# Optimization experiments

Hardware: AMD Instinct MI355X
Metric: run time of the kernel (lower is better)

## Reference

```python
import jax, jax.numpy as jnp
import numpy as np

B = 65536
NFIELD = 20
NFEAT = 1_000_000
SQL_NEMB = 10
DATA_NEMB = 10
HID = 64
K = 16
C = 2
COL_CARD = NFIELD + NFEAT + 1
GATE_IN = NFIELD * SQL_NEMB
EXP_IN = NFIELD * DATA_NEMB
EPS = 1e-5


def _bn(x, g, b, m, v):
    # eval-mode BatchNorm1d: affine normalize with running stats
    return (x - m) * jax.lax.rsqrt(v + EPS) * g + b


def setup_inputs() -> dict:
    key = jax.random.key(0)
    ks = jax.random.split(key, 12)
    n = lambda k, s, sc=0.05: jax.random.normal(k, s, jnp.float32) * sc
    return {
        "x": jax.random.randint(ks[0], (B, NFIELD), 0, NFEAT, dtype=jnp.int32),
        "sql": jax.random.randint(ks[1], (B, NFIELD), 0, COL_CARD, dtype=jnp.int32),
        "input_table": n(ks[2], (NFEAT, DATA_NEMB)),
        "sql_table": n(ks[3], (COL_CARD, SQL_NEMB)),
        "gate_w1": n(ks[4], (GATE_IN, HID)), "gate_b1": jnp.zeros((HID,), jnp.float32),
        "gate_w2": n(ks[5], (HID, K)), "gate_b2": jnp.zeros((K,), jnp.float32),
        "e_w1": n(ks[6], (K, EXP_IN, HID)), "e_b1": jnp.zeros((K, HID), jnp.float32),
        "e_g1": jnp.ones((K, HID), jnp.float32), "e_beta1": jnp.zeros((K, HID), jnp.float32),
        "e_m1": jnp.zeros((K, HID), jnp.float32), "e_v1": jnp.ones((K, HID), jnp.float32),
        "e_w2": n(ks[7], (K, HID, HID)), "e_b2": jnp.zeros((K, HID), jnp.float32),
        "e_g2": jnp.ones((K, HID), jnp.float32), "e_beta2": jnp.zeros((K, HID), jnp.float32),
        "e_m2": jnp.zeros((K, HID), jnp.float32), "e_v2": jnp.ones((K, HID), jnp.float32),
        "p_w1": n(ks[8], (HID, HID)), "p_b1": jnp.zeros((HID,), jnp.float32),
        "p_g": jnp.ones((HID,), jnp.float32), "p_beta": jnp.zeros((HID,), jnp.float32),
        "p_m": jnp.zeros((HID,), jnp.float32), "p_v": jnp.ones((HID,), jnp.float32),
        "p_w2": n(ks[9], (HID, 1)), "p_b2": jnp.zeros((1,), jnp.float32),
    }


def reference(x, sql, input_table, sql_table, gate_w1, gate_b1, gate_w2, gate_b2,
              e_w1, e_b1, e_g1, e_beta1, e_m1, e_v1,
              e_w2, e_b2, e_g2, e_beta2, e_m2, e_v2,
              p_w1, p_b1, p_g, p_beta, p_m, p_v, p_w2, p_b2):
    Bn = x.shape[0]
    # embedding lookups -> flatten fields
    x_emb = input_table[x].reshape(Bn, -1)      # [B, nfield*data_nemb]
    sql_emb = sql_table[sql].reshape(Bn, -1)    # [B, nfield*sql_nemb]
    # gate network (MLP + softmax) over K experts
    gh = jax.nn.relu(sql_emb @ gate_w1 + gate_b1)
    scores = jax.nn.softmax(gh @ gate_w2 + gate_b2, axis=-1)  # [B, K]
    # sparse top-C selection, scatter back to dense gates, renormalize
    topv, topi = jax.lax.top_k(scores, C)
    gates = jnp.zeros_like(scores).at[jnp.arange(Bn)[:, None], topi].set(topv)
    gates = gates / (gates.sum(-1, keepdims=True) + 1e-9)     # [B, K]
    # expert compute (dense-equivalent; zero gates kill unselected experts)
    h1 = jax.nn.relu(_bn(jnp.einsum('bi,kih->kbh', x_emb, e_w1) + e_b1[:, None, :],
                         e_g1[:, None, :], e_beta1[:, None, :], e_m1[:, None, :], e_v1[:, None, :]))
    h2 = jax.nn.relu(_bn(jnp.einsum('kbh,khg->kbg', h1, e_w2) + e_b2[:, None, :],
                         e_g2[:, None, :], e_beta2[:, None, :], e_m2[:, None, :], e_v2[:, None, :]))
    y = jnp.einsum('bk,kbh->bh', gates, h2)                   # combine [B, HID]
    # load-balance loss: cv^2 of expert importance
    importance = gates.sum(0)
    loss = importance.var() / (importance.mean() ** 2 + 1e-10)
    # predict head
    ph = jax.nn.relu(_bn(y @ p_w1 + p_b1, p_g, p_beta, p_m, p_v))
    out = (ph @ p_w2 + p_b2).squeeze(-1)                      # [B]
    return out, loss
```

## Files before the change

### kernel.cpp

```cpp
#include <hip/hip_runtime.h>
#include <hip/hip_bf16.h>

#define BB 65536
#define NFIELD 20
#define HID 64
#define KEXP 16
#define EPS 1e-5f
#define KPAD 224
#define NKS 7
#define NBLK_GATE 1024
#define NBX_EXP 40
#define TSTR 228

typedef __attribute__((ext_vector_type(8))) short v8s;
typedef __attribute__((ext_vector_type(4))) float v4f;

#define OFF_GCNT 0
#define OFF_SC1 64
#define OFF_SH1 1088
#define OFF_SC2 2112
#define OFF_SH2 3136
#define OFF_SCP 4160
#define OFF_SHP 4224
#define OFF_IMP 4288
#define OFF_LIDX 20672
#define OFF_LW  1069248
#define OFF_W1T 2117824
#define OFF_GW1T 2232512
#define OFF_W2T 2239680
#define OFF_PW1T 2272448
#define OFF_XEMB 2274496
#define OFF_HS 9614640

__device__ __forceinline__ unsigned short f2bf(float f) {
    unsigned int u = __float_as_uint(f);
    unsigned int r = (u + 0x7FFFu + ((u >> 16) & 1u)) >> 16;
    return (unsigned short)r;
}
__device__ __forceinline__ float bf2f(unsigned short u) {
    unsigned int t = ((unsigned int)u) << 16;
    return __uint_as_float(t);
}
__device__ __forceinline__ unsigned int pack2(float a, float b) {
    return (unsigned int)f2bf(a) | ((unsigned int)f2bf(b) << 16);
}

__global__ __launch_bounds__(256) void k_prep(
    const float* __restrict__ ew1, const float* __restrict__ ew2,
    const float* __restrict__ gw1, const float* __restrict__ pw1,
    const float* __restrict__ eb1, const float* __restrict__ eg1,
    const float* __restrict__ ebe1, const float* __restrict__ em1,
    const float* __restrict__ ev1,
    const float* __restrict__ eb2, const float* __restrict__ eg2,
    const float* __restrict__ ebe2, const float* __restrict__ em2,
    const float* __restrict__ ev2,
    const float* __restrict__ pb1, const float* __restrict__ pg,
    const float* __restrict__ pbe, const float* __restrict__ pm,
    const float* __restrict__ pv,
    float* __restrict__ wsf, int* __restrict__ gcnt,
    unsigned short* __restrict__ w1t, unsigned short* __restrict__ gw1t,
    unsigned short* __restrict__ w2t, unsigned short* __restrict__ pw1t)
{
    int gid = blockIdx.x * 256 + threadIdx.x;
    if (gid < 229376) {
        int k = gid / 14336, r = gid % 14336, c = r / KPAD, t = r % KPAD;
        w1t[gid] = (t < 200) ? f2bf(ew1[((size_t)k * 200 + t) * HID + c]) : 0;
    } else if (gid < 229376 + 14336) {
        int g2 = gid - 229376; int c = g2 / KPAD, t = g2 % KPAD;
        gw1t[g2] = (t < 200) ? f2bf(gw1[t * HID + c]) : 0;
    } else if (gid < 243712 + 65536) {
        int g2 = gid - 243712; int k = g2 / 4096, r = g2 % 4096, g = r / 64, i = r % 64;
        w2t[g2] = f2bf(ew2[((size_t)k * 64 + i) * 64 + g]);
    } else if (gid < 309248 + 4096) {
        int g2 = gid - 309248; int g = g2 / 64, i = g2 % 64;
        pw1t[g2] = f2bf(pw1[i * 64 + g]);
    } else if (gid < 313344 + 1024) {
        int t = gid - 313344;
        float rs1 = rsqrtf(ev1[t] + EPS) * eg1[t];
        wsf[OFF_SC1 + t] = rs1;
        wsf[OFF_SH1 + t] = fmaf(eb1[t] - em1[t], rs1, ebe1[t]);
        float rs2 = rsqrtf(ev2[t] + EPS) * eg2[t];
        wsf[OFF_SC2 + t] = rs2;
        wsf[OFF_SH2 + t] = fmaf(eb2[t] - em2[t], rs2, ebe2[t]);
    } else if (gid < 314368 + 64) {
        int t = gid - 314368;
        float rs = rsqrtf(pv[t] + EPS) * pg[t];
        wsf[OFF_SCP + t] = rs;
        wsf[OFF_SHP + t] = fmaf(pb1[t] - pm[t], rs, pbe[t]);
    } else if (gid < 314432 + 16) {
        gcnt[gid - 314432] = 0;
    }
}

__global__ __launch_bounds__(256) void k_gate(
    const int* __restrict__ x, const int* __restrict__ sql,
    const float* __restrict__ itab, const float* __restrict__ stab,
    const unsigned short* __restrict__ gw1t,
    const float* __restrict__ gb1, const float* __restrict__ gw2,
    const float* __restrict__ gb2,
    unsigned short* __restrict__ xembT,
    int* __restrict__ lidx, float* __restrict__ lw,
    int* __restrict__ gcnt, float* __restrict__ imp_part)
{
    __shared__ unsigned short tile[64][TSTR];
    __shared__ float s_imp[KEXP];
    __shared__ int s_cnt[KEXP];
    __shared__ int s_base[KEXP];
    unsigned short (*Hg)[80] = (unsigned short (*)[80])&tile[0][0];
    int tid = threadIdx.x;
    int wid = tid >> 6, l = tid & 63;
    int m = l & 15, q = l >> 4;
    int b0 = blockIdx.x * 64;

    if (tid < KEXP) { s_imp[tid] = 0.f; s_cnt[tid] = 0; }
    for (int t = tid; t < 64 * 12; t += 256) {
        int r = t / 12, c2 = t % 12;
        *(unsigned int*)&tile[r][200 + 2 * c2] = 0;
    }
    {
        uint4 z4 = {0u, 0u, 0u, 0u};
        if (tid < 192) {
            int row = tid / 3, j = tid % 3;
            *(uint4*)((char*)(xembT + (size_t)(b0 + row) * KPAD) + 400 + 16 * j) = z4;
        }
    }
#pragma unroll
    for (int rr = 0; rr < 5; ++rr) {
        int r = tid + rr * 256;
        int lb = r / NFIELD, f = r % NFIELD;
        int sidx = sql[(size_t)(b0 + lb) * NFIELD + f];
        int xidx = x[(size_t)(b0 + lb) * NFIELD + f];
        const float* srow = stab + (size_t)sidx * 10;
        const float* xrow = itab + (size_t)xidx * 10;
        float2 s0 = *(const float2*)(srow + 0);
        float2 s1 = *(const float2*)(srow + 2);
        float2 s2 = *(const float2*)(srow + 4);
        float2 s3 = *(const float2*)(srow + 6);
        float2 s4 = *(const float2*)(srow + 8);
        float2 x0 = *(const float2*)(xrow + 0);
        float2 x1 = *(const float2*)(xrow + 2);
        float2 x2 = *(const float2*)(xrow + 4);
        float2 x3 = *(const float2*)(xrow + 6);
        float2 x4 = *(const float2*)(xrow + 8);
        unsigned int* lrow = (unsigned int*)&tile[lb][f * 10];
        lrow[0] = pack2(s0.x, s0.y);
        lrow[1] = pack2(s1.x, s1.y);
        lrow[2] = pack2(s2.x, s2.y);
        lrow[3] = pack2(s3.x, s3.y);
        lrow[4] = pack2(s4.x, s4.y);
        unsigned int* grow = (unsigned int*)(xembT + (size_t)(b0 + lb) * KPAD + f * 10);
        grow[0] = pack2(x0.x, x0.y);
        grow[1] = pack2(x1.x, x1.y);
        grow[2] = pack2(x2.x, x2.y);
        grow[3] = pack2(x3.x, x3.y);
        grow[4] = pack2(x4.x, x4.y);
    }
    __syncthreads();

    v4f zero4 = {0.f, 0.f, 0.f, 0.f};
    v4f acc[4];
#pragma unroll
    for (int a = 0; a < 4; ++a) acc[a] = zero4;
    const unsigned short* Bb = gw1t + (wid * 16 + m) * KPAD + q * 8;
#pragma unroll
    for (int Ks = 0; Ks < NKS; ++Ks) {
        v8s bv = *(const v8s*)(Bb + Ks * 32);
        v8s a[4];
#pragma unroll
        for (int Mt = 0; Mt < 4; ++Mt)
            a[Mt] = *(const v8s*)&tile[Mt * 16 + m][Ks * 32 + q * 8];
#pragma unroll
        for (int Mt = 0; Mt < 4; ++Mt)
            acc[Mt] = __builtin_amdgcn_mfma_f32_16x16x32_bf16(a[Mt], bv, acc[Mt], 0, 0, 0);
    }
    __syncthreads();

    int c = wid * 16 + m;
    float bias = gb1[c];
#pragma unroll
    for (int Mt = 0; Mt < 4; ++Mt)
#pragma unroll
        for (int j = 0; j < 4; ++j) {
            int item = Mt * 16 + q * 4 + j;
            float v = fmaxf(acc[Mt][j] + bias, 0.f);
            Hg[item][c ^ ((item & 7) << 3)] = f2bf(v);
        }
    __syncthreads();

    if (wid == 0) {
        float z[KEXP];
#pragma unroll
        for (int j = 0; j < KEXP; ++j) z[j] = gb2[j];
#pragma unroll
        for (int u = 0; u < 8; ++u) {
            v8s hv = *(const v8s*)&Hg[l][(u * 8) ^ ((l & 7) << 3)];
#pragma unroll
            for (int e = 0; e < 8; ++e) {
                int h = u * 8 + e;
                float g = bf2f((unsigned short)hv[e]);
#pragma unroll
                for (int j = 0; j < KEXP; ++j) z[j] = fmaf(g, gw2[h * KEXP + j], z[j]);
            }
        }
        float mm = z[0];
#pragma unroll
        for (int j = 1; j < KEXP; ++j) mm = fmaxf(mm, z[j]);
        float s = 0.f;
#pragma unroll
        for (int j = 0; j < KEXP; ++j) s += expf(z[j] - mm);
        int i0 = 0; float m0 = z[0];
#pragma unroll
        for (int j = 1; j < KEXP; ++j) if (z[j] > m0) { m0 = z[j]; i0 = j; }
        int i1 = (i0 == 0) ? 1 : 0; float m1 = -3.4e38f;
#pragma unroll
        for (int j = 0; j < KEXP; ++j) if (j != i0 && z[j] > m1) { m1 = z[j]; i1 = j; }
        float v0 = expf(m0 - mm) / s, v1 = expf(m1 - mm) / s;
        float inv = 1.f / (v0 + v1 + 1e-9f);
        float w0 = v0 * inv, w1 = v1 * inv;

        atomicAdd(&s_imp[i0], w0);
        atomicAdd(&s_imp[i1], w1);
        int o0 = atomicAdd(&s_cnt[i0], 1);
        int o1 = atomicAdd(&s_cnt[i1], 1);
        __syncthreads();
        if (l < KEXP) s_base[l] = atomicAdd(&gcnt[l], s_cnt[l]);
        __syncthreads();
        int b = b0 + l;
        int p0 = i0 * BB + s_base[i0] + o0;
        lidx[p0] = (b << 1);     lw[p0] = w0;
        int p1 = i1 * BB + s_base[i1] + o1;
        lidx[p1] = (b << 1) | 1; lw[p1] = w1;
    } else {
        __syncthreads();
        __syncthreads();
    }
    __syncthreads();
    if (tid < KEXP) imp_part[blockIdx.x * KEXP + tid] = s_imp[tid];
}

__global__ void k_pad(const int* __restrict__ gcnt, int* __restrict__ lidx,
                      float* __restrict__ lw)
{
    int k = blockIdx.x;
    int n = gcnt[k];
    int ne = (n + 63) & ~63;
    for (int i = n + threadIdx.x; i < ne; i += 64) {
        lidx[k * BB + i] = 2 * BB;
        lw[k * BB + i] = 0.f;
    }
}

__global__ __launch_bounds__(256) void k_loss(const float* __restrict__ imp_part,
                                              float* __restrict__ out)
{
    __shared__ double sred[16][17];
    __shared__ double simp[KEXP];
    int tid = threadIdx.x;
    int j = tid & 15, g = tid >> 4;
    double s = 0.0;
    for (int blk = g; blk < NBLK_GATE; blk += 16) s += (double)imp_part[blk * KEXP + j];
    sred[g][j] = s;
    __syncthreads();
    if (tid < KEXP) {
        double t = 0.0;
#pragma unroll
        for (int gg = 0; gg < 16; ++gg) t += sred[gg][tid];
        simp[tid] = t;
    }
    __syncthreads();
    if (tid == 0) {
        double mean = 0.0;
        for (int jj = 0; jj < KEXP; ++jj) mean += simp[jj];
        mean /= KEXP;
        double var = 0.0;
        for (int jj = 0; jj < KEXP; ++jj) { double d = simp[jj] - mean; var += d * d; }
        var /= KEXP;
        out[BB] = (float)(var / (mean * mean + 1e-10));
    }
}

__global__ __launch_bounds__(256, 2) void k_exp(
    const unsigned short* __restrict__ xembT,
    const unsigned short* __restrict__ w1t, const unsigned short* __restrict__ w2t,
    const float* __restrict__ sc1, const float* __restrict__ sh1,
    const float* __restrict__ sc2, const float* __restrict__ sh2,
    const int* __restrict__ lidx, const float* __restrict__ lw,
    const int* __restrict__ gcnt, unsigned short* __restrict__ hs)
{
    __shared__ unsigned short Hl[4][64][80];
    int k = blockIdx.y;
    int tid = threadIdx.x;
    int wid = tid >> 6, l = tid & 63;
    int m = l & 15, q = l >> 4;
    int n = gcnt[k];
    int ne = (n + 63) & ~63;
    const unsigned short* W1 = w1t + (size_t)k * 64 * KPAD + m * KPAD + q * 8;
    const unsigned short* W2 = w2t + (size_t)k * 64 * 64 + m * 64 + q * 8;
    float sc1v[4], sh1v[4], sc2v[4], sh2v[4];
#pragma unroll
    for (int Nt = 0; Nt < 4; ++Nt) {
        int c = Nt * 16 + m;
        sc1v[Nt] = sc1[k * HID + c]; sh1v[Nt] = sh1[k * HID + c];
        sc2v[Nt] = sc2[k * HID + c]; sh2v[Nt] = sh2[k * HID + c];
    }
    v4f zero4 = {0.f, 0.f, 0.f, 0.f};

    for (int it0 = (blockIdx.x * 4 + wid) * 64; it0 < ne; it0 += NBX_EXP * 256) {
        int eA[4];
#pragma unroll
        for (int Mt = 0; Mt < 4; ++Mt) eA[Mt] = lidx[k * BB + it0 + Mt * 16 + m];
        v4f acc1[4][4];
#pragma unroll
        for (int a = 0; a < 4; ++a)
#pragma unroll
            for (int c = 0; c < 4; ++c) acc1[a][c] = zero4;
#pragma unroll
        for (int Ks = 0; Ks < NKS; ++Ks) {
            v8s a[4], b[4];
#pragma unroll
            for (int Mt = 0; Mt < 4; ++Mt)
                a[Mt] = *(const v8s*)(xembT + (size_t)(eA[Mt] >> 1) * KPAD + Ks * 32 + q * 8);
#pragma unroll
            for (int Nt = 0; Nt < 4; ++Nt)
                b[Nt] = *(const v8s*)(W1 + Nt * 16 * KPAD + Ks * 32);
#pragma unroll
            for (int Mt = 0; Mt < 4; ++Mt)
#pragma unroll
                for (int Nt = 0; Nt < 4; ++Nt)
                    acc1[Mt][Nt] = __builtin_amdgcn_mfma_f32_16x16x32_bf16(a[Mt], b[Nt], acc1[Mt][Nt], 0, 0, 0);
        }
#pragma unroll
        for (int Nt = 0; Nt < 4; ++Nt) {
            int c = Nt * 16 + m;
#pragma unroll
            for (int Mt = 0; Mt < 4; ++Mt)
#pragma unroll
                for (int j = 0; j < 4; ++j) {
                    int item = Mt * 16 + q * 4 + j;
                    float v = fmaxf(fmaf(acc1[Mt][Nt][j], sc1v[Nt], sh1v[Nt]), 0.f);
                    Hl[wid][item][c ^ ((item & 7) << 3)] = f2bf(v);
                }
        }
        v4f acc2[4][4];
#pragma unroll
        for (int a = 0; a < 4; ++a)
#pragma unroll
            for (int c = 0; c < 4; ++c) acc2[a][c] = zero4;
#pragma unroll
        for (int Ks = 0; Ks < 2; ++Ks) {
            v8s a[4], b[4];
#pragma unroll
            for (int Mt = 0; Mt < 4; ++Mt)
                a[Mt] = *(const v8s*)&Hl[wid][Mt * 16 + m][(Ks * 32 + q * 8) ^ ((m & 7) << 3)];
#pragma unroll
            for (int Nt = 0; Nt < 4; ++Nt)
                b[Nt] = *(const v8s*)(W2 + Nt * 16 * 64 + Ks * 32);
#pragma unroll
            for (int Mt = 0; Mt < 4; ++Mt)
#pragma unroll
                for (int Nt = 0; Nt < 4; ++Nt)
                    acc2[Mt][Nt] = __builtin_amdgcn_mfma_f32_16x16x32_bf16(a[Mt], b[Nt], acc2[Mt][Nt], 0, 0, 0);
        }
#pragma unroll
        for (int Mt = 0; Mt < 4; ++Mt) {
            float4 wC = *(const float4*)&lw[k * BB + it0 + Mt * 16 + q * 4];
            float wj[4] = {wC.x, wC.y, wC.z, wC.w};
#pragma unroll
            for (int Nt = 0; Nt < 4; ++Nt) {
                int c = Nt * 16 + m;
#pragma unroll
                for (int j = 0; j < 4; ++j) {
                    int item = Mt * 16 + q * 4 + j;
                    float v = wj[j] * fmaxf(fmaf(acc2[Mt][Nt][j], sc2v[Nt], sh2v[Nt]), 0.f);
                    Hl[wid][item][c ^ ((item & 7) << 3)] = f2bf(v);
                }
            }
        }
        int eo = lidx[k * BB + it0 + l];
        unsigned short* hrow = hs + (size_t)eo * HID;
#pragma unroll
        for (int u = 0; u < 8; ++u)
            *(v8s*)(hrow + u * 8) = *(const v8s*)&Hl[wid][l][(u * 8) ^ ((l & 7) << 3)];
    }
}

__global__ __launch_bounds__(256, 2) void k_head(
    const unsigned short* __restrict__ hs, const unsigned short* __restrict__ pw1t,
    const float* __restrict__ scp, const float* __restrict__ shp,
    const float* __restrict__ pw2, const float* __restrict__ pb2,
    float* __restrict__ out)
{
    int tid = threadIdx.x;
    int wid = tid >> 6, l = tid & 63;
    int m = l & 15, q = l >> 4;
    int it0 = blockIdx.x * 256 + wid * 64;
    float scv[4], shv[4], w2v[4];
#pragma unroll
    for (int Nt = 0; Nt < 4; ++Nt) {
        int c = Nt * 16 + m;
        scv[Nt] = scp[c]; shv[Nt] = shp[c]; w2v[Nt] = pw2[c];
    }
    v4f zero4 = {0.f, 0.f, 0.f, 0.f};
    v4f acc[4][4];
#pragma unroll
    for (int a = 0; a < 4; ++a)
#pragma unroll
        for (int c = 0; c < 4; ++c) acc[a][c] = zero4;

#pragma unroll
    for (int Ks = 0; Ks < 2; ++Ks) {
        v8s a[4], b[4];
#pragma unroll
        for (int Mt = 0; Mt < 4; ++Mt) {
            int bi = it0 + Mt * 16 + m;
            const unsigned short* r0 = hs + (size_t)(2 * bi) * HID + Ks * 32 + q * 8;
            v8s u0 = *(const v8s*)r0;
            v8s u1 = *(const v8s*)(r0 + HID);
            v8s av;
#pragma unroll
            for (int e = 0; e < 8; ++e) {
                float f = bf2f((unsigned short)u0[e]) + bf2f((unsigned short)u1[e]);
                av[e] = (short)f2bf(f);
            }
            a[Mt] = av;
        }
#pragma unroll
        for (int Nt = 0; Nt < 4; ++Nt)
            b[Nt] = *(const v8s*)(pw1t + (Nt * 16 + m) * HID + Ks * 32 + q * 8);
#pragma unroll
        for (int Mt = 0; Mt < 4; ++Mt)
#pragma unroll
            for (int Nt = 0; Nt < 4; ++Nt)
                acc[Mt][Nt] = __builtin_amdgcn_mfma_f32_16x16x32_bf16(a[Mt], b[Nt], acc[Mt][Nt], 0, 0, 0);
    }
    float pb2v = pb2[0];
#pragma unroll
    for (int Mt = 0; Mt < 4; ++Mt) {
#pragma unroll
        for (int j = 0; j < 4; ++j) {
            float po = 0.f;
#pragma unroll
            for (int Nt = 0; Nt < 4; ++Nt) {
                float ph = fmaxf(fmaf(acc[Mt][Nt][j], scv[Nt], shv[Nt]), 0.f);
                po = fmaf(ph, w2v[Nt], po);
            }
            po += __shfl_xor(po, 1);
            po += __shfl_xor(po, 2);
            po += __shfl_xor(po, 4);
            po += __shfl_xor(po, 8);
            if (m == 0) out[it0 + Mt * 16 + q * 4 + j] = po + pb2v;
        }
    }
}

extern "C" void kernel_launch(void* const* d_in, const int* in_sizes, int n_in,
                              void* d_out, int out_size, void* d_ws, size_t ws_size,
                              hipStream_t stream) {
    const int*   x     = (const int*)d_in[0];
    const int*   sql   = (const int*)d_in[1];
    const float* itab  = (const float*)d_in[2];
    const float* stab  = (const float*)d_in[3];
    const float* gw1   = (const float*)d_in[4];
    const float* gb1   = (const float*)d_in[5];
    const float* gw2   = (const float*)d_in[6];
    const float* gb2   = (const float*)d_in[7];
    const float* ew1   = (const float*)d_in[8];
    const float* eb1   = (const float*)d_in[9];
    const float* eg1   = (const float*)d_in[10];
    const float* ebe1  = (const float*)d_in[11];
    const float* em1   = (const float*)d_in[12];
    const float* ev1   = (const float*)d_in[13];
    const float* ew2   = (const float*)d_in[14];
    const float* eb2   = (const float*)d_in[15];
    const float* eg2   = (const float*)d_in[16];
    const float* ebe2  = (const float*)d_in[17];
    const float* em2   = (const float*)d_in[18];
    const float* ev2   = (const float*)d_in[19];
    const float* pw1   = (const float*)d_in[20];
    const float* pb1   = (const float*)d_in[21];
    const float* pg    = (const float*)d_in[22];
    const float* pbe   = (const float*)d_in[23];
    const float* pm    = (const float*)d_in[24];
    const float* pv    = (const float*)d_in[25];
    const float* pw2   = (const float*)d_in[26];
    const float* pb2   = (const float*)d_in[27];

    float* wsf = (float*)d_ws;
    int*   wsi = (int*)d_ws;
    int*   gcnt = wsi + OFF_GCNT;
    float* sc1 = wsf + OFF_SC1;
    float* sh1 = wsf + OFF_SH1;
    float* sc2 = wsf + OFF_SC2;
    float* sh2 = wsf + OFF_SH2;
    float* scp = wsf + OFF_SCP;
    float* shp = wsf + OFF_SHP;
    float* imp = wsf + OFF_IMP;
    int*   lidx = wsi + OFF_LIDX;
    float* lw  = wsf + OFF_LW;
    unsigned short* w1t   = (unsigned short*)(wsf + OFF_W1T);
    unsigned short* gw1t  = (unsigned short*)(wsf + OFF_GW1T);
    unsigned short* w2t   = (unsigned short*)(wsf + OFF_W2T);
    unsigned short* pw1t  = (unsigned short*)(wsf + OFF_PW1T);
    unsigned short* xembT = (unsigned short*)(wsf + OFF_XEMB);
    unsigned short* hs    = (unsigned short*)(wsf + OFF_HS);
    float* out = (float*)d_out;

    k_prep<<<1229, 256, 0, stream>>>(ew1, ew2, gw1, pw1,
                                     eb1, eg1, ebe1, em1, ev1,
                                     eb2, eg2, ebe2, em2, ev2,
                                     pb1, pg, pbe, pm, pv,
                                     wsf, gcnt, w1t, gw1t, w2t, pw1t);
    k_gate<<<NBLK_GATE, 256, 0, stream>>>(x, sql, itab, stab, gw1t, gb1, gw2, gb2,
                                          xembT, lidx, lw, gcnt, imp);
    k_loss<<<1, 256, 0, stream>>>(imp, out);
    k_pad<<<16, 64, 0, stream>>>(gcnt, lidx, lw);
    dim3 ge(NBX_EXP, KEXP);
    k_exp<<<ge, 256, 0, stream>>>(xembT, w1t, w2t, sc1, sh1, sc2, sh2,
                                  lidx, lw, gcnt, hs);
    k_head<<<256, 256, 0, stream>>>(hs, pw1t, scp, shp, pw2, pb2, out);
}
```

Before: 151.3 us.

## Double gate block to eight waves, widen expert grid, shrink expert LDS

The gate kernel now runs 512 threads per block. Each of the eight waves computes one 16-row M tile against two 16-column N tiles, instead of four waves each covering all M tiles for one N tile, and the gather loop is re-strided with a bounds guard. The expert kernel grid doubles along x, and its per-wave hidden staging buffer drops from 80 to 64 columns to cut LDS use. The aim is more parallelism and latency hiding in the gather and MFMA phases. The risks are extra sync cost, possible LDS bank conflicts from the unpadded stride, and any hidden code that still assumes 256 threads.

```diff
diff --git a/kernel.cpp b/kernel.cpp
--- a/kernel.cpp
+++ b/kernel.cpp
@@ -9,7 +9,7 @@
 #define KPAD 224
 #define NKS 7
 #define NBLK_GATE 1024
-#define NBX_EXP 40
+#define NBX_EXP 80
 #define TSTR 228
 
 typedef __attribute__((ext_vector_type(8))) short v8s;
@@ -92,7 +92,7 @@
     }
 }
 
-__global__ __launch_bounds__(256) void k_gate(
+__global__ __launch_bounds__(512, 8) void k_gate(
     const int* __restrict__ x, const int* __restrict__ sql,
     const float* __restrict__ itab, const float* __restrict__ stab,
     const unsigned short* __restrict__ gw1t,
@@ -113,7 +113,7 @@
     int b0 = blockIdx.x * 64;
 
     if (tid < KEXP) { s_imp[tid] = 0.f; s_cnt[tid] = 0; }
-    for (int t = tid; t < 64 * 12; t += 256) {
+    for (int t = tid; t < 64 * 12; t += 512) {
         int r = t / 12, c2 = t % 12;
         *(unsigned int*)&tile[r][200 + 2 * c2] = 0;
     }
@@ -125,66 +125,67 @@
         }
     }
 #pragma unroll
-    for (int rr = 0; rr < 5; ++rr) {
-        int r = tid + rr * 256;
-        int lb = r / NFIELD, f = r % NFIELD;
-        int sidx = sql[(size_t)(b0 + lb) * NFIELD + f];
-        int xidx = x[(size_t)(b0 + lb) * NFIELD + f];
-        const float* srow = stab + (size_t)sidx * 10;
-        const float* xrow = itab + (size_t)xidx * 10;
-        float2 s0 = *(const float2*)(srow + 0);
-        float2 s1 = *(const float2*)(srow + 2);
-        float2 s2 = *(const float2*)(srow + 4);
-        float2 s3 = *(const float2*)(srow + 6);
-        float2 s4 = *(const float2*)(srow + 8);
-        float2 x0 = *(const float2*)(xrow + 0);
-        float2 x1 = *(const float2*)(xrow + 2);
-        float2 x2 = *(const float2*)(xrow + 4);
-        float2 x3 = *(const float2*)(xrow + 6);
-        float2 x4 = *(const float2*)(xrow + 8);
-        unsigned int* lrow = (unsigned int*)&tile[lb][f * 10];
-        lrow[0] = pack2(s0.x, s0.y);
-        lrow[1] = pack2(s1.x, s1.y);
-        lrow[2] = pack2(s2.x, s2.y);
-        lrow[3] = pack2(s3.x, s3.y);
-        lrow[4] = pack2(s4.x, s4.y);
-        unsigned int* grow = (unsigned int*)(xembT + (size_t)(b0 + lb) * KPAD + f * 10);
-        grow[0] = pack2(x0.x, x0.y);
-        grow[1] = pack2(x1.x, x1.y);
-        grow[2] = pack2(x2.x, x2.y);
-        grow[3] = pack2(x3.x, x3.y);
-        grow[4] = pack2(x4.x, x4.y);
+    for (int rr = 0; rr < 3; ++rr) {
+        int r = tid + rr * 512;
+        if (r < 64 * NFIELD) {
+            int lb = r / NFIELD, f = r % NFIELD;
+            int sidx = sql[(size_t)(b0 + lb) * NFIELD + f];
+            int xidx = x[(size_t)(b0 + lb) * NFIELD + f];
+            const float* srow = stab + (size_t)sidx * 10;
+            const float* xrow = itab + (size_t)xidx * 10;
+            float2 s0 = *(const float2*)(srow + 0);
+            float2 s1 = *(const float2*)(srow + 2);
+            float2 s2 = *(const float2*)(srow + 4);
+            float2 s3 = *(const float2*)(srow + 6);
+            float2 s4 = *(const float2*)(srow + 8);
+            float2 x0 = *(const float2*)(xrow + 0);
+            float2 x1 = *(const float2*)(xrow + 2);
+            float2 x2 = *(const float2*)(xrow + 4);
+            float2 x3 = *(const float2*)(xrow + 6);
+            float2 x4 = *(const float2*)(xrow + 8);
+            unsigned int* lrow = (unsigned int*)&tile[lb][f * 10];
+            lrow[0] = pack2(s0.x, s0.y);
+            lrow[1] = pack2(s1.x, s1.y);
+            lrow[2] = pack2(s2.x, s2.y);
+            lrow[3] = pack2(s3.x, s3.y);
+            lrow[4] = pack2(s4.x, s4.y);
+            unsigned int* grow = (unsigned int*)(xembT + (size_t)(b0 + lb) * KPAD + f * 10);
+            grow[0] = pack2(x0.x, x0.y);
+            grow[1] = pack2(x1.x, x1.y);
+            grow[2] = pack2(x2.x, x2.y);
+            grow[3] = pack2(x3.x, x3.y);
+            grow[4] = pack2(x4.x, x4.y);
+        }
     }
     __syncthreads();
 
+    int Mt = wid >> 1, Ntb = (wid & 1) * 2;
     v4f zero4 = {0.f, 0.f, 0.f, 0.f};
-    v4f acc[4];
-#pragma unroll
-    for (int a = 0; a < 4; ++a) acc[a] = zero4;
-    const unsigned short* Bb = gw1t + (wid * 16 + m) * KPAD + q * 8;
+    v4f acc0 = zero4, acc1 = zero4;
+    const unsigned short* Bb0 = gw1t + (Ntb * 16 + m) * KPAD + q * 8;
+    const unsigned short* Bb1 = gw1t + ((Ntb + 1) * 16 + m) * KPAD + q * 8;
 #pragma unroll
     for (int Ks = 0; Ks < NKS; ++Ks) {
-        v8s bv = *(const v8s*)(Bb + Ks * 32);
-        v8s a[4];
-#pragma unroll
-        for (int Mt = 0; Mt < 4; ++Mt)
-            a[Mt] = *(const v8s*)&tile[Mt * 16 + m][Ks * 32 + q * 8];
-#pragma unroll
-        for (int Mt = 0; Mt < 4; ++Mt)
-            acc[Mt] = __builtin_amdgcn_mfma_f32_16x16x32_bf16(a[Mt], bv, acc[Mt], 0, 0, 0);
+        v8s av = *(const v8s*)&tile[Mt * 16 + m][Ks * 32 + q * 8];
+        v8s b0v = *(const v8s*)(Bb0 + Ks * 32);
+        v8s b1v = *(const v8s*)(Bb1 + Ks * 32);
+        acc0 = __builtin_amdgcn_mfma_f32_16x16x32_bf16(av, b0v, acc0, 0, 0, 0);
+        acc1 = __builtin_amdgcn_mfma_f32_16x16x32_bf16(av, b1v, acc1, 0, 0, 0);
     }
     __syncthreads();
 
-    int c = wid * 16 + m;
-    float bias = gb1[c];
-#pragma unroll
-    for (int Mt = 0; Mt < 4; ++Mt)
+#pragma unroll
+    for (int t = 0; t < 2; ++t) {
+        int c = (Ntb + t) * 16 + m;
+        float bias = gb1[c];
+        v4f av = t ? acc1 : acc0;
 #pragma unroll
         for (int j = 0; j < 4; ++j) {
             int item = Mt * 16 + q * 4 + j;
-            float v = fmaxf(acc[Mt][j] + bias, 0.f);
+            float v = fmaxf(av[j] + bias, 0.f);
             Hg[item][c ^ ((item & 7) << 3)] = f2bf(v);
         }
+    }
     __syncthreads();
 
     if (wid == 0) {
@@ -287,7 +288,7 @@
     const int* __restrict__ lidx, const float* __restrict__ lw,
     const int* __restrict__ gcnt, unsigned short* __restrict__ hs)
 {
-    __shared__ unsigned short Hl[4][64][80];
+    __shared__ unsigned short Hl[4][64][64];
     int k = blockIdx.y;
     int tid = threadIdx.x;
     int wid = tid >> 6, l = tid & 63;
@@ -510,7 +511,7 @@
                                      eb2, eg2, ebe2, em2, ev2,
                                      pb1, pg, pbe, pm, pv,
                                      wsf, gcnt, w1t, gw1t, w2t, pw1t);
-    k_gate<<<NBLK_GATE, 256, 0, stream>>>(x, sql, itab, stab, gw1t, gb1, gw2, gb2,
+    k_gate<<<NBLK_GATE, 512, 0, stream>>>(x, sql, itab, stab, gw1t, gb1, gw2, gb2,
                                           xembT, lidx, lw, gcnt, imp);
     k_loss<<<1, 256, 0, stream>>>(imp, out);
     k_pad<<<16, 64, 0, stream>>>(gcnt, lidx, lw);
```

After: 157.2 us. 3.9% more time.

## Batch embedding gathers with wide nontemporal loads and double expert grid width

Applied to the files above, without the earlier changes.

The embedding gather is restructured so each thread first loads all five index pairs, then issues every table-row load, and only then converts to bf16 and stores. This raises the number of outstanding memory requests and replaces float2 loads with 16-byte and 8-byte vector loads marked nontemporal. Global stores of the data embedding are merged into a 16-byte store plus one 4-byte store. The expert kernel's block-count constant also doubles from 40 to 80. The vector accesses sit at 40-byte and 20-byte strides, so they rely on unaligned wide global access being tolerated, and holding all loaded rows at once raises register pressure.

```diff
diff --git a/kernel.cpp b/kernel.cpp
--- a/kernel.cpp
+++ b/kernel.cpp
@@ -9,11 +9,12 @@
 #define KPAD 224
 #define NKS 7
 #define NBLK_GATE 1024
-#define NBX_EXP 40
+#define NBX_EXP 80
 #define TSTR 228
 
 typedef __attribute__((ext_vector_type(8))) short v8s;
 typedef __attribute__((ext_vector_type(4))) float v4f;
+typedef __attribute__((ext_vector_type(2))) float v2f;
 
 #define OFF_GCNT 0
 #define OFF_SC1 64
@@ -124,36 +125,54 @@
             *(uint4*)((char*)(xembT + (size_t)(b0 + row) * KPAD) + 400 + 16 * j) = z4;
         }
     }
-#pragma unroll
-    for (int rr = 0; rr < 5; ++rr) {
-        int r = tid + rr * 256;
-        int lb = r / NFIELD, f = r % NFIELD;
-        int sidx = sql[(size_t)(b0 + lb) * NFIELD + f];
-        int xidx = x[(size_t)(b0 + lb) * NFIELD + f];
-        const float* srow = stab + (size_t)sidx * 10;
-        const float* xrow = itab + (size_t)xidx * 10;
-        float2 s0 = *(const float2*)(srow + 0);
-        float2 s1 = *(const float2*)(srow + 2);
-        float2 s2 = *(const float2*)(srow + 4);
-        float2 s3 = *(const float2*)(srow + 6);
-        float2 s4 = *(const float2*)(srow + 8);
-        float2 x0 = *(const float2*)(xrow + 0);
-        float2 x1 = *(const float2*)(xrow + 2);
-        float2 x2 = *(const float2*)(xrow + 4);
-        float2 x3 = *(const float2*)(xrow + 6);
-        float2 x4 = *(const float2*)(xrow + 8);
-        unsigned int* lrow = (unsigned int*)&tile[lb][f * 10];
-        lrow[0] = pack2(s0.x, s0.y);
-        lrow[1] = pack2(s1.x, s1.y);
-        lrow[2] = pack2(s2.x, s2.y);
-        lrow[3] = pack2(s3.x, s3.y);
-        lrow[4] = pack2(s4.x, s4.y);
-        unsigned int* grow = (unsigned int*)(xembT + (size_t)(b0 + lb) * KPAD + f * 10);
-        grow[0] = pack2(x0.x, x0.y);
-        grow[1] = pack2(x1.x, x1.y);
-        grow[2] = pack2(x2.x, x2.y);
-        grow[3] = pack2(x3.x, x3.y);
-        grow[4] = pack2(x4.x, x4.y);
+    {
+        int sidx[5], xidx[5];
+#pragma unroll
+        for (int rr = 0; rr < 5; ++rr) {
+            int r = tid + rr * 256;
+            sidx[rr] = sql[(size_t)b0 * NFIELD + r];
+            xidx[rr] = x[(size_t)b0 * NFIELD + r];
+        }
+        v4f sA[5], sB[5]; v2f sC[5];
+        v4f xA[5], xB[5]; v2f xC[5];
+#pragma unroll
+        for (int rr = 0; rr < 5; ++rr) {
+            const float* srow = stab + (size_t)sidx[rr] * 10;
+            sA[rr] = __builtin_nontemporal_load((const v4f*)(srow + 0));
+            sB[rr] = __builtin_nontemporal_load((const v4f*)(srow + 4));
+            sC[rr] = __builtin_nontemporal_load((const v2f*)(srow + 8));
+        }
+#pragma unroll
+        for (int rr = 0; rr < 5; ++rr) {
+            const float* xrow = itab + (size_t)xidx[rr] * 10;
+            xA[rr] = __builtin_nontemporal_load((const v4f*)(xrow + 0));
+            xB[rr] = __builtin_nontemporal_load((const v4f*)(xrow + 4));
+            xC[rr] = __builtin_nontemporal_load((const v2f*)(xrow + 8));
+        }
+#pragma unroll
+        for (int rr = 0; rr < 5; ++rr) {
+            int r = tid + rr * 256;
+            int lb = r / NFIELD, f = r % NFIELD;
+            unsigned int* lrow = (unsigned int*)&tile[lb][f * 10];
+            lrow[0] = pack2(sA[rr].x, sA[rr].y);
+            lrow[1] = pack2(sA[rr].z, sA[rr].w);
+            lrow[2] = pack2(sB[rr].x, sB[rr].y);
+            lrow[3] = pack2(sB[rr].z, sB[rr].w);
+            lrow[4] = pack2(sC[rr].x, sC[rr].y);
+        }
+#pragma unroll
+        for (int rr = 0; rr < 5; ++rr) {
+            int r = tid + rr * 256;
+            int lb = r / NFIELD, f = r % NFIELD;
+            unsigned int* grow = (unsigned int*)(xembT + (size_t)(b0 + lb) * KPAD + f * 10);
+            uint4 g0;
+            g0.x = pack2(xA[rr].x, xA[rr].y);
+            g0.y = pack2(xA[rr].z, xA[rr].w);
+            g0.z = pack2(xB[rr].x, xB[rr].y);
+            g0.w = pack2(xB[rr].z, xB[rr].w);
+            *(uint4*)grow = g0;
+            grow[4] = pack2(xC[rr].x, xC[rr].y);
+        }
     }
     __syncthreads();
 
```

New measurement: 228.3 us. 1.51x slower.
